# Kernel tuning notes

Measured on AMD Instinct MI355X. Metric: run time of the kernel, lower is better.

The kernel has to match this reference:

```python
import jax, jax.numpy as jnp
import numpy as np

# ---- static hyperparameters (mirror init_kwargs) ----
L_MAX = 3
N_MAX_L = [8, 6, 4, 2]            # radial basis size per l (precomputer.n_max_l)
N_CHANNELS = 32                   # num_element_channels
K_MAX_L = [n * N_CHANNELS for n in N_MAX_L]   # [256, 192, 128, 64]
SH_SIZES = [2 * l + 1 for l in range(L_MAX + 1)]  # [1,3,5,7]
MP_SCALING = 0.1
NU_SCALING = 0.1
NU_MAX = 2                        # max_correlation_order_per_layer
N_LAYERS = 2                      # num_message_passing_layers

# Fixed CG coupling tensors for all valid (l1, l2, L) with |l1-l2|<=L<=min(l1+l2, L_MAX).
# (Deterministic stand-ins for real Clebsch-Gordan coefficients; same sparsity/coupling
# structure and identical in fwd and fwdbwd modules.)
_rng = np.random.RandomState(0)
CG = {}
for _l1 in range(L_MAX + 1):
    for _l2 in range(L_MAX + 1):
        for _L in range(abs(_l1 - _l2), min(_l1 + _l2, L_MAX) + 1):
            CG[(_l1, _l2, _L)] = jnp.asarray(
                (_rng.randn(2 * _l1 + 1, 2 * _l2 + 1, 2 * _L + 1) * 0.2).astype(np.float32))


def split_l(x, sizes):
    out, i = [], 0
    for s in sizes:
        out.append(x[:, i:i + s])
        i += s
    return out


def embed_centers(feats, emb):
    # feats[l]: [N, 2l+1, n_l*C]; multiply channel block c by per-atom embedding emb[:, c]
    C = emb.shape[1]
    out = []
    for f in feats:
        n, m, k = f.shape
        out.append((f.reshape(n, m, k // C, C) * emb[:, None, None, :]).reshape(n, m, k))
    return out


def tensor_product(A, B):
    # per-atom CG tensor product, channel-aligned with truncation to min k
    n = A[0].shape[0]
    out = [jnp.zeros((n, 2 * L + 1, K_MAX_L[L]), A[0].dtype) for L in range(L_MAX + 1)]
    for (l1, l2, L), cg in CG.items():
        kk = min(K_MAX_L[l1], K_MAX_L[l2], K_MAX_L[L])
        t = jnp.einsum('nak,nbk,abM->nMk', A[l1][:, :, :kk], B[l2][:, :, :kk], cg)
        out[L] = out[L].at[:, :, :kk].add(t)
    return out


def cg_iterate(feats):
    # CGIterator: nu_max-1 iterated tensor products with residual accumulation
    g = feats
    for _ in range(NU_MAX - 1):
        tp = tensor_product(g, feats)
        g = [g[l] + NU_SCALING * tp[l] for l in range(L_MAX + 1)]
    return g


def invariant_mp(rb_l, sh_l, centers, emb_nbr, n_atoms):
    # spherical expansion: scatter rb x sh x neighbor-embedding over pairs -> centers
    out = []
    for l in range(L_MAX + 1):
        # [P, 2l+1, n_l, C] -> [P, 2l+1, k_l]
        msg = sh_l[l][:, :, None, None] * rb_l[l][:, None, :, None] * emb_nbr[:, None, None, :]
        msg = msg.reshape(msg.shape[0], 2 * l + 1, -1)
        out.append(MP_SCALING * jax.ops.segment_sum(msg, centers, num_segments=n_atoms))
    return out


def equivariant_mp(rb_l, sh_l, centers, neighbors, feats, n_atoms):
    # pair messages: CG-couple radially weighted SH edge features with neighbor features
    edge = [sh_l[l] * rb_l[l].sum(-1, keepdims=True) for l in range(L_MAX + 1)]  # [P, 2l+1]
    out = [jnp.zeros((n_atoms, 2 * L + 1, K_MAX_L[L]), feats[0].dtype) for L in range(L_MAX + 1)]
    for (l1, l2, L), cg in CG.items():
        kk = min(K_MAX_L[l2], K_MAX_L[L])
        w = jnp.einsum('pa,abM->pbM', edge[l1], cg)        # [P, 2l2+1, 2L+1]
        fg = feats[l2][neighbors, :, :kk]                   # gather: [P, 2l2+1, kk]
        msg = jnp.einsum('pbM,pbk->pMk', w, fg)             # [P, 2L+1, kk]
        out[L] = out[L].at[:, :, :kk].add(
            MP_SCALING * jax.ops.segment_sum(msg, centers, num_segments=n_atoms))
    return out


def setup_inputs() -> dict:
    key = jax.random.key(0)
    ks = jax.random.split(key, 8)
    N, P = 5000, 100000
    return {
        'sh': jax.random.normal(ks[0], (P, sum(SH_SIZES)), dtype=jnp.float32),
        'rb': jax.random.uniform(ks[1], (P, sum(N_MAX_L)), dtype=jnp.float32),
        'emb_table': jax.random.normal(ks[2], (4, N_CHANNELS), dtype=jnp.float32),
        'w_energy': jax.random.normal(ks[3], (K_MAX_L[0], 1), dtype=jnp.float32) * 0.05,
        'b_energy': jax.random.normal(ks[4], (1,), dtype=jnp.float32),
        'species_idx': jax.random.randint(ks[5], (N,), 0, 4, dtype=jnp.int32),
        'centers': jax.random.randint(ks[6], (P,), 0, N, dtype=jnp.int32),
        'neighbors': jax.random.randint(ks[7], (P,), 0, N, dtype=jnp.int32),
    }


def reference(sh, rb, emb_table, w_energy, b_energy, species_idx, centers, neighbors):
    n_atoms = species_idx.shape[0]
    sh_l = split_l(sh * NU_SCALING, SH_SIZES)   # nu_scaling applied to spherical harmonics
    rb_l = split_l(rb, N_MAX_L)
    center_emb = emb_table[species_idx]          # [N, C]
    emb_nbr = center_emb[neighbors]              # [P, C]
    # invariant message passing -> spherical expansion, then first CG iteration
    feats = invariant_mp(rb_l, sh_l, centers, emb_nbr, n_atoms)
    feats = cg_iterate(feats)
    # remaining equivariant message-passing layers
    for _ in range(N_LAYERS - 1):
        ef = embed_centers(feats, center_emb)
        mp = equivariant_mp(rb_l, sh_l, centers, neighbors, ef, n_atoms)
        feats = cg_iterate(mp)
    feats = embed_centers(feats, center_emb)
    energies = feats[0] @ w_energy + b_energy    # [N, 1, 1]
    return energies
```

## Files before the change

kernel.cpp:

```cpp
#include <hip/hip_runtime.h>
#include <vector>
#include <cmath>
#include <cstdint>

constexpr int KLc[4]  = {256,192,128,64};
constexpr int NMLc[4] = {8,6,4,2};
constexpr int SHBc[5] = {0,1,4,9,16};
constexpr int RBBc[5] = {0,8,14,18,20};
constexpr int FBc[5]  = {0,256,832,1472,1920};
constexpr int NCMB = 34, CGTOT = 3436, FTOT = 1920;

struct Combos { int l1[NCMB], l2[NCMB], L[NCMB], cgoff[NCMB], kk[NCMB]; };
constexpr Combos make_combos(){
  Combos c{}; int n=0, cg=0;
  for(int a=0;a<=3;a++)for(int b=0;b<=3;b++){
    int lo=a>b?a-b:b-a, hi=(a+b<3)?(a+b):3;
    for(int L=lo;L<=hi;L++){
      c.l1[n]=a; c.l2[n]=b; c.L[n]=L; c.cgoff[n]=cg;
      int mx=a>b?a:b; if(L>mx) mx=L; c.kk[n]=KLc[mx];
      cg+=(2*a+1)*(2*b+1)*(2*L+1); n++;
    }
  }
  return c;
}
constexpr Combos CB = make_combos();
static_assert(CB.cgoff[NCMB-1] + 7*7*7 == CGTOT, "cg size");

struct Grp { int cnt[4]; int list[4][12]; };
constexpr Grp make_Lg(){ Grp g{}; for(int i=0;i<NCMB;i++){ int L=CB.L[i]; g.list[L][g.cnt[L]++]=i; } return g; }
constexpr Grp LG = make_Lg();

struct Rows { int sh[64], rb[64], off[64]; };
constexpr Rows make_rows(){ Rows r{}; int i=0;
  for(int l=0;l<4;l++)for(int m=0;m<2*l+1;m++)for(int n=0;n<NMLc[l];n++){
    r.sh[i]=SHBc[l]+m; r.rb[i]=RBBc[l]+n; r.off[i]=FBc[l]+m*KLc[l]+n*32; i++; }
  for(;i<64;i++){ r.sh[i]=0; r.rb[i]=0; r.off[i]=0; }
  return r; }
constexpr Rows RWS = make_rows();

constexpr int NSL=425, NG=16, RPAD=149;
constexpr int JB=48, DEPTH=8;
static_assert(JB % DEPTH == 0, "slot rotation alignment");
constexpr int NTILE=30;

constexpr int iabs_(int x){ return x<0?-x:x; }
__host__ __device__ constexpr bool sl_valid(int l1,int l2,int kt){ return l2<=3-kt && iabs_(l1-l2)<=3-kt; }

__host__ __device__ constexpr int rb_base(int kt,int l1,int l2){
  int base=0;
  for(int p=0;p<4;p++)for(int q=0;q<4;q++){
    if(p==l1 && q==l2) return base;
    if(sl_valid(p,q,kt)) base += (2*p+1)*(2*q+1);
  }
  return base;
}

struct EqTab {
  short       srow[NG][32];
  signed char sph [NG][32];
  int nr[NG];
  short roff[NG][2];
  int total;
};
constexpr EqTab make_eqtab(){
  EqTab T{};
  for(int g=0;g<NG;g++){
    for(int s=0;s<32;s++){ T.srow[g][s]=-1; T.sph[g][s]=-1; }
    T.nr[g]=0; T.roff[g][0]=0; T.roff[g][1]=0;
  }
  int tl2[NTILE]{}, tkt[NTILE]{}, tbb[NTILE]{}, tsz[NTILE]{}; int nt=0;
  for(int l2=0;l2<4;l2++)for(int kt=0;kt<4-l2;kt++)for(int b=0;b<2*l2+1;b++){
    int sz=0;
    for(int l1=0;l1<4;l1++) if(sl_valid(l1,l2,kt)) sz+=2*l1+1;
    tl2[nt]=l2; tkt[nt]=kt; tbb[nt]=b; tsz[nt]=sz; nt++;
  }
  bool used[NTILE]{}; int gload[NG]{}; int gcnt[NG]{}; int gt[NG][2]{};
  for(int it=0; it<nt; it++){
    int best=-1;
    for(int i=0;i<nt;i++) if(!used[i] && (best<0 || tsz[i]>tsz[best])) best=i;
    used[best]=true;
    int g=-1;
    for(int j=0;j<NG;j++) if(gcnt[j]<2 && (g<0 || gload[j]<gload[g])) g=j;
    gt[g][gcnt[g]]=best; gcnt[g]++; gload[g]+=tsz[best];
  }
  int total=0;
  for(int g=0;g<NG;g++){
    T.nr[g]=gcnt[g];
    for(int tk=0;tk<gcnt[g];tk++){
      const int ti=gt[g][tk];
      const int l2=tl2[ti], kt=tkt[ti], b=tbb[ti];
      T.roff[g][tk]=(short)(FBc[l2]+b*KLc[l2]+kt*64);
      for(int i=0;i<16;i++){
        const int l1=(i==0)?0:(i<4)?1:(i<9)?2:3;
        const int aa=i-SHBc[l1];
        if(!sl_valid(l1,l2,kt)) continue;
        const int s=tk*16+i;
        const int rbi=rb_base(kt,l1,l2)+aa*(2*l2+1)+b;
        int ph, sr;
        if(kt==0){ if(l1<=2){ ph=0; sr=rbi; } else { ph=1; sr=rbi-144; } }
        else { ph=kt+1; sr=rbi; }
        T.sph[g][s]=(signed char)ph; T.srow[g][s]=(short)sr;
        total++;
      }
    }
    if(gcnt[g]==1) T.roff[g][1]=T.roff[g][0];
  }
  T.total=total;
  return T;
}
constexpr EqTab ET = make_eqtab();
static_assert(ET.total==NSL, "slice count");
constexpr bool chk_srow(){ for(int g=0;g<NG;g++) for(int s=0;s<32;s++) if(ET.srow[g][s]>=RPAD) return false; return true; }
static_assert(chk_srow(), "stage rows fit RPAD");

struct RoffA { int r0[NG]; int r1[NG]; };
constexpr RoffA make_roffa(){ RoffA R{}; for(int g=0;g<NG;g++){ R.r0[g]=ET.roff[g][0]; R.r1[g]=ET.roff[g][1]; } return R; }
constexpr RoffA RFA = make_roffa();

struct CAsg { int cnt[NG]; unsigned char ci[NG][8]; };
constexpr CAsg make_casg(){
  CAsg C{}; bool used[NCMB]{}; int load[NG]{};
  for(int it=0; it<NCMB; it++){
    int best=-1, bc=-1;
    for(int i=0;i<NCMB;i++) if(!used[i]){
      int c=(2*CB.l1[i]+1)*(2*CB.l2[i]+1)*(2*CB.L[i]+1);
      if(c>bc){bc=c;best=i;}
    }
    used[best]=true;
    int g=0; for(int j=1;j<NG;j++) if(load[j]<load[g]) g=j;
    C.ci[g][C.cnt[g]++]=(unsigned char)best; load[g]+=bc;
  }
  return C;
}
constexpr CAsg CA = make_casg();
constexpr bool chk_ca(){ for(int g=0;g<NG;g++) if(CA.cnt[g]>8) return false; return true; }
static_assert(chk_ca(), "CA cap");

__host__ __device__ constexpr bool combo_in_phase(int ci,int ph){
  int l1=CB.l1[ci], l2=CB.l2[ci], L=CB.L[ci];
  if(ph==0) return l1<=2;
  if(ph==1) return l1==3;
  int kt=ph-1;
  return (l2<=3-kt) && (L<=3-kt);
}
__host__ __device__ constexpr int phase_kt(int ph){ return ph<=1?0:ph-1; }
__host__ __device__ constexpr int phase_rbadj(int ph){ return ph==1?144:0; }

namespace nprng {
struct MT {
  uint32_t mt[624]; int mti; bool has_g; double g;
  void seed(uint32_t s){ for(int i=0;i<624;i++){ mt[i]=s; s=1812433253u*(s^(s>>30))+(uint32_t)i+1u; } mti=624; has_g=false; g=0.0; }
  uint32_t u32(){
    if(mti>=624){
      for(int i=0;i<624;i++){
        uint32_t y=(mt[i]&0x80000000u)|(mt[(i+1)%624]&0x7fffffffu);
        mt[i]=mt[(i+397)%624]^(y>>1)^((y&1u)?0x9908b0dfu:0u);
      }
      mti=0;
    }
    uint32_t y=mt[mti++];
    y^=y>>11; y^=(y<<7)&0x9d2c5680u; y^=(y<<15)&0xefc60000u; y^=y>>18;
    return y;
  }
  double dbl(){ uint32_t a=u32()>>5, b=u32()>>6; return (a*67108864.0+b)/9007199254740992.0; }
  double gauss(){
    if(has_g){ has_g=false; return g; }
    double f,x1,x2,r2;
    do{ x1=2.0*dbl()-1.0; x2=2.0*dbl()-1.0; r2=x1*x1+x2*x2; }while(r2>=1.0||r2==0.0);
    f=sqrt(-2.0*log(r2)/r2);
    g=f*x1; has_g=true; return f*x2;
  }
};
}
static std::vector<float> build_cg(){
  nprng::MT r; r.seed(0);
  std::vector<float> v; v.reserve(CGTOT);
  for(int l1=0;l1<=3;l1++)for(int l2=0;l2<=3;l2++){
    int lo = l1>l2? l1-l2 : l2-l1;
    int hi = (l1+l2<3)? (l1+l2) : 3;
    for(int L=lo;L<=hi;L++){
      int n=(2*l1+1)*(2*l2+1)*(2*L+1);
      for(int i=0;i<n;i++) v.push_back((float)(r.gauss()*0.2));
    }
  }
  return v;
}

__global__ __launch_bounds__(256) void k_cemb(const float* __restrict__ emb_table,
    const int* __restrict__ species, float* __restrict__ cemb, int* __restrict__ counts, int N){
  int i = blockIdx.x*256 + threadIdx.x;
  if(i < N) counts[i] = 0;
  if(i < N*32){ int n = i>>5, c = i&31; cemb[i] = emb_table[species[n]*32 + c]; }
}

__global__ __launch_bounds__(256) void k_hist(const int* __restrict__ centers, int* counts, int P){
  int i = blockIdx.x*256 + threadIdx.x;
  if(i < P) atomicAdd(&counts[centers[i]], 1);
}

__global__ __launch_bounds__(256) void k_scan(const int* __restrict__ counts,
    int* __restrict__ offsets, int* __restrict__ cursor, int N){
  __shared__ int part[256];
  const int t = threadIdx.x;
  const int CH = (N + 255)/256;
  const int lo = t*CH;
  int hi = (t+1)*CH; if(hi > N) hi = N;
  int s = 0;
  for(int i=lo;i<hi;i++) s += counts[i];
  part[t] = s; __syncthreads();
  const int own = s;
  for(int d=1; d<256; d<<=1){
    int v = (t>=d)? part[t-d] : 0;
    __syncthreads();
    part[t] += v;
    __syncthreads();
  }
  int run = part[t] - own;
  for(int i=lo;i<hi;i++){ offsets[i]=run; cursor[i]=run; run += counts[i]; }
  if(t==255) offsets[N] = part[255];
}

__global__ __launch_bounds__(256) void k_scatter(const int* __restrict__ centers,
    int* cursor, int* __restrict__ perm, int P){
  int i = blockIdx.x*256 + threadIdx.x;
  if(i < P){ int c = centers[i]; int pos = atomicAdd(&cursor[c], 1); perm[pos] = i; }
}

__global__ __launch_bounds__(256) void k_permute(const float* __restrict__ sh,
    const float* __restrict__ rb, const int* __restrict__ nbrs, const int* __restrict__ perm,
    float* __restrict__ edge_p, int* __restrict__ nbrp, int P){
  int u = blockIdx.x*256 + threadIdx.x;
  int pos = u>>4, i = u&15;
  if(pos >= P) return;
  int p = perm[pos];
  if(i==0) nbrp[pos] = nbrs[p];
  int l = (i==0)?0:(i<4)?1:(i<9)?2:3;
  float s=0.f;
  for(int n=RBBc[l]; n<RBBc[l+1]; n++) s += rb[p*20+n];
  edge_p[(size_t)pos*16+i] = sh[p*16+i]*0.1f*s;
}

__global__ __launch_bounds__(256) void k_inv(const float* __restrict__ sh, const float* __restrict__ rb,
    const float* __restrict__ cemb, const int* __restrict__ nbrs, const int* __restrict__ offsets,
    const int* __restrict__ perm, float* __restrict__ feats){
  const int a = blockIdx.x, t = threadIdx.x;
  __shared__ float sh_s[8][16], rb_s[8][20], emb_s[8][32], shrb_s[8][60];
  const int c = t & 31, rg = t >> 5;
  float acc[8];
  #pragma unroll
  for(int j=0;j<8;j++) acc[j] = 0.f;
  const int beg = offsets[a], cnt = offsets[a+1]-beg;
  for(int jb=0; jb<cnt; jb+=8){
    __syncthreads();
    for(int u=t; u<8*36; u+=256){
      int j=u/36, i=u-36*j;
      if(jb+j<cnt){
        int p=perm[beg+jb+j];
        if(i<16) sh_s[j][i]=sh[p*16+i]*0.1f;
        else     rb_s[j][i-16]=rb[p*20+i-16];
      }
    }
    for(int u=t; u<8*32; u+=256){
      int j=u>>5, i=u&31;
      if(jb+j<cnt){ int nb=nbrs[perm[beg+jb+j]]; emb_s[j][i]=cemb[(size_t)nb*32+i]; }
    }
    __syncthreads();
    for(int u=t; u<8*60; u+=256){
      int j=u/60, r=u-60*j;
      if(jb+j<cnt) shrb_s[j][r] = sh_s[j][RWS.sh[r]] * rb_s[j][RWS.rb[r]];
    }
    __syncthreads();
    const int jm = (cnt-jb<8)?(cnt-jb):8;
    for(int j=0;j<jm;j++){
      const float e = emb_s[j][c];
      #pragma unroll
      for(int q=0;q<8;q++){ int r=rg+8*q; if(r<60) acc[q]=fmaf(shrb_s[j][r], e, acc[q]); }
    }
  }
  #pragma unroll
  for(int q=0;q<8;q++){
    int r = rg + 8*q;
    if(r < 60) feats[(size_t)a*FTOT + RWS.off[r] + c] = 0.1f * acc[q];
  }
}

__device__ __forceinline__ float cg_u(const float* __restrict__ cg, int idx){
  return cg[__builtin_amdgcn_readfirstlane(idx)];
}
__global__ __launch_bounds__(256) void k_tp(float* __restrict__ feats, const float* __restrict__ cg){
  const int a = blockIdx.x, t = threadIdx.x;
  __shared__ float f_s[FTOT];
  float* fa = feats + (size_t)a*FTOT;
  for(int i=t;i<FTOT;i+=256)  f_s[i]  = fa[i];
  __syncthreads();
  #pragma unroll
  for(int L=0; L<4; L++){
    const int KLL = KLc[L], nL = 2*L+1;
    const int nel = nL*KLL;
    for(int e=t; e<nel; e+=256){
      const int M = e / KLL, k = e - M*KLL;
      float acc = 0.f;
      #pragma unroll
      for(int gi=0; gi<LG.cnt[L]; gi++){
        const int ci = LG.list[L][gi];
        const int l1 = CB.l1[ci], l2 = CB.l2[ci];
        if(k < CB.kk[ci]){
          const int n2 = 2*l2+1;
          #pragma unroll
          for(int aa=0; aa<2*l1+1; aa++){
            const float Av = f_s[FBc[l1] + aa*KLc[l1] + k];
            #pragma unroll
            for(int b=0; b<n2; b++)
              acc += cg_u(cg, CB.cgoff[ci] + (aa*n2+b)*nL + M) * (Av * f_s[FBc[l2] + b*KLc[l2] + k]);
          }
        }
      }
      fa[FBc[L] + M*KLL + k] = f_s[FBc[L] + M*KLL + k] + 0.1f*acc;
    }
  }
}

template<int G,int PH,int U>
__device__ __forceinline__ void contract_combos(const float* __restrict__ stageT,
    float* __restrict__ out_s, const float* __restrict__ cg, int lane){
  if constexpr (U < CA.cnt[G]) {
    constexpr int ci = CA.ci[G][U];
    if constexpr (combo_in_phase(ci,PH)) {
      constexpr int l1=CB.l1[ci], l2=CB.l2[ci], L=CB.L[ci];
      constexpr int n1=2*l1+1, n2=2*l2+1, nL=2*L+1;
      constexpr int kt=phase_kt(PH);
      constexpr int rbase = rb_base(kt,l1,l2) - phase_rbadj(PH);
      float oa[nL];
      #pragma unroll
      for(int M=0;M<nL;M++) oa[M]=0.f;
      #pragma unroll
      for(int aa=0;aa<n1;aa++){
        #pragma unroll
        for(int b=0;b<n2;b++){
          const float sv = stageT[lane*RPAD + rbase + aa*n2 + b];
          #pragma unroll
          for(int M=0;M<nL;M++)
            oa[M] = fmaf(cg[CB.cgoff[ci] + (aa*n2+b)*nL + M], sv, oa[M]);
        }
      }
      #pragma unroll
      for(int M=0;M<nL;M++)
        atomicAdd(&out_s[FBc[L] + M*KLc[L] + kt*64 + lane], oa[M]);
    }
    contract_combos<G,PH,U+1>(stageT,out_s,cg,lane);
  }
}

template<int G,int PH>
__device__ __forceinline__ void eq_phase(const float* acc, float* stageT, float* out_s,
    const float* __restrict__ cg, int lane){
  __syncthreads();
  #pragma unroll
  for(int s=0;s<32;s++){
    if(ET.sph[G][s]==PH) stageT[lane*RPAD + ET.srow[G][s]] = acc[s];
  }
  __syncthreads();
  contract_combos<G,PH,0>(stageT,out_s,cg,lane);
}

template<int G>
__device__ __forceinline__ void eq_phases(const float* acc, float* stageT, float* out_s,
    const float* __restrict__ cg, int lane){
  eq_phase<G,0>(acc,stageT,out_s,cg,lane);
  eq_phase<G,1>(acc,stageT,out_s,cg,lane);
  eq_phase<G,2>(acc,stageT,out_s,cg,lane);
  eq_phase<G,3>(acc,stageT,out_s,cg,lane);
  eq_phase<G,4>(acc,stageT,out_s,cg,lane);
}

__device__ __forceinline__ void eq_load_pair(float* fg, float& ce, int nb, int lane,
    int ro0, int ro1, const float* __restrict__ featsA, const float* __restrict__ cemb){
  ce = cemb[(size_t)nb*32 + (lane&31)];
  const float* fp = featsA + (size_t)nb*FTOT + lane;
  fg[0] = fp[ro0];
  fg[1] = fp[ro1];
}

__device__ __forceinline__ void eq_compute_pair(float* acc, const float* fg, float ce,
    const float* edge_row){
  float ed[16];
  #pragma unroll
  for(int q=0;q<4;q++){
    float4 v = *(const float4*)(edge_row + q*4);
    ed[q*4]=v.x; ed[q*4+1]=v.y; ed[q*4+2]=v.z; ed[q*4+3]=v.w;
  }
  const float f0 = fg[0]*ce, f1 = fg[1]*ce;
  #pragma unroll
  for(int i=0;i<16;i++) acc[i]    = fmaf(ed[i], f0, acc[i]);
  #pragma unroll
  for(int i=0;i<16;i++) acc[16+i] = fmaf(ed[i], f1, acc[16+i]);
}

__global__ __launch_bounds__(1024,4) void k_eq2(const float* __restrict__ edge_p,
    const int* __restrict__ nbrp, const float* __restrict__ cemb,
    const int* __restrict__ offsets, const float* __restrict__ featsA,
    float* __restrict__ featsB, const float* __restrict__ cg){
  __shared__ float stageT[64*RPAD];
  __shared__ float out_s[FTOT];
  __shared__ float edge_s[JB*16];
  __shared__ int   nb_s[JB];
  const int a = blockIdx.x, t = threadIdx.x, lane = t&63, g = t>>6;

  float acc[32];
  #pragma unroll
  for(int s=0;s<32;s++) acc[s]=0.f;
  for(int i=t;i<FTOT;i+=1024) out_s[i]=0.f;
  const int beg = offsets[a], cnt = offsets[a+1]-beg;
  const int ro0 = __builtin_amdgcn_readfirstlane(RFA.r0[g]);
  const int ro1 = __builtin_amdgcn_readfirstlane(RFA.r1[g]);

  float fgS[DEPTH][2]; float ceS[DEPTH];
  #pragma unroll
  for(int s=0;s<DEPTH;s++){
    int nb = (s<cnt)? nbrp[beg+s] : 0;
    eq_load_pair(fgS[s], ceS[s], nb, lane, ro0, ro1, featsA, cemb);
  }
  for(int jb=0; jb<cnt; jb+=JB){
    __syncthreads();
    if(t < JB*16){
      int j = t>>4;
      if(jb+j < cnt) edge_s[t] = edge_p[(size_t)(beg+jb)*16 + t];
    }
    if(t < JB) nb_s[t] = (jb+t < cnt) ? nbrp[beg+jb+t] : 0;
    __syncthreads();
    const int jm = (cnt-jb<JB)?(cnt-jb):JB;
    for(int j=0;j<jm;j+=DEPTH){
      #pragma unroll
      for(int s=0;s<DEPTH;s++){
        if(j+s < jm){
          eq_compute_pair(acc, fgS[s], ceS[s], edge_s + (j+s)*16);
          int q = jb+j+s+DEPTH;
          int nb = (q<cnt) ? ((q-jb<JB)? nb_s[q-jb] : nbrp[beg+q]) : 0;
          eq_load_pair(fgS[s], ceS[s], nb, lane, ro0, ro1, featsA, cemb);
        }
      }
    }
  }

  switch(g){
    case 0:  eq_phases<0 >(acc,stageT,out_s,cg,lane); break;
    case 1:  eq_phases<1 >(acc,stageT,out_s,cg,lane); break;
    case 2:  eq_phases<2 >(acc,stageT,out_s,cg,lane); break;
    case 3:  eq_phases<3 >(acc,stageT,out_s,cg,lane); break;
    case 4:  eq_phases<4 >(acc,stageT,out_s,cg,lane); break;
    case 5:  eq_phases<5 >(acc,stageT,out_s,cg,lane); break;
    case 6:  eq_phases<6 >(acc,stageT,out_s,cg,lane); break;
    case 7:  eq_phases<7 >(acc,stageT,out_s,cg,lane); break;
    case 8:  eq_phases<8 >(acc,stageT,out_s,cg,lane); break;
    case 9:  eq_phases<9 >(acc,stageT,out_s,cg,lane); break;
    case 10: eq_phases<10>(acc,stageT,out_s,cg,lane); break;
    case 11: eq_phases<11>(acc,stageT,out_s,cg,lane); break;
    case 12: eq_phases<12>(acc,stageT,out_s,cg,lane); break;
    case 13: eq_phases<13>(acc,stageT,out_s,cg,lane); break;
    case 14: eq_phases<14>(acc,stageT,out_s,cg,lane); break;
    default: eq_phases<15>(acc,stageT,out_s,cg,lane); break;
  }
  __syncthreads();
  float* ob = featsB + (size_t)a*FTOT;
  for(int i=t;i<FTOT;i+=1024) ob[i] = 0.1f*out_s[i];
}

__global__ __launch_bounds__(256) void k_energy(const float* __restrict__ feats,
    const float* __restrict__ cemb, const float* __restrict__ wE, const float* __restrict__ bE,
    float* __restrict__ out, int N){
  const int wid = threadIdx.x >> 6, lane = threadIdx.x & 63;
  const int a = blockIdx.x*4 + wid;
  if(a >= N) return;
  const float e = cemb[(size_t)a*32 + (lane & 31)];
  float s = 0.f;
  for(int k=lane; k<256; k+=64) s += feats[(size_t)a*FTOT + k] * e * wE[k];
  #pragma unroll
  for(int off=32; off; off>>=1) s += __shfl_down(s, off, 64);
  if(lane == 0) out[a] = s + bE[0];
}

extern "C" void kernel_launch(void* const* d_in, const int* in_sizes, int n_in,
                              void* d_out, int out_size, void* d_ws, size_t ws_size,
                              hipStream_t stream){
  const float* sh        = (const float*)d_in[0];
  const float* rb        = (const float*)d_in[1];
  const float* emb_table = (const float*)d_in[2];
  const float* wE        = (const float*)d_in[3];
  const float* bE        = (const float*)d_in[4];
  const int*   species   = (const int*)d_in[5];
  const int*   centers   = (const int*)d_in[6];
  const int*   nbrs      = (const int*)d_in[7];
  const int N = in_sizes[5];
  const int P = in_sizes[6];

  char* ws = (char*)d_ws; size_t off = 0;
  auto carve = [&](size_t bytes)->void*{
    void* p = ws + off; off = (off + bytes + 255) & ~(size_t)255; return p;
  };
  float* cg_d    = (float*)carve((size_t)CGTOT*4);
  float* cemb    = (float*)carve((size_t)N*32*4);
  int*   counts  = (int*)  carve((size_t)N*4);
  int*   offsets = (int*)  carve((size_t)(N+1)*4);
  int*   cursor  = (int*)  carve((size_t)N*4);
  int*   perm    = (int*)  carve((size_t)P*4);
  float* edge_pd = (float*)carve((size_t)P*16*4);
  int*   nbrp    = (int*)  carve((size_t)P*4);
  float* featsA  = (float*)carve((size_t)N*FTOT*4);
  float* featsB  = (float*)carve((size_t)N*FTOT*4);
  (void)ws_size; (void)n_in; (void)out_size;

  static const std::vector<float> cg_host = build_cg();
  hipMemcpyAsync(cg_d, cg_host.data(), (size_t)CGTOT*4, hipMemcpyHostToDevice, stream);

  k_cemb   <<<(N*32 + 255)/256, 256, 0, stream>>>(emb_table, species, cemb, counts, N);
  k_hist   <<<(P + 255)/256,    256, 0, stream>>>(centers, counts, P);
  k_scan   <<<1,                256, 0, stream>>>(counts, offsets, cursor, N);
  k_scatter<<<(P + 255)/256,    256, 0, stream>>>(centers, cursor, perm, P);
  k_permute<<<(P*16 + 255)/256, 256, 0, stream>>>(sh, rb, nbrs, perm, edge_pd, nbrp, P);
  k_inv    <<<N,                256, 0, stream>>>(sh, rb, cemb, nbrs, offsets, perm, featsA);
  k_tp     <<<N,                256, 0, stream>>>(featsA, cg_d);
  k_eq2    <<<N,               1024, 0, stream>>>(edge_pd, nbrp, cemb, offsets, featsA, featsB, cg_d);
  k_tp     <<<N,                256, 0, stream>>>(featsB, cg_d);
  k_energy <<<(N + 3)/4,        256, 0, stream>>>(featsB, cemb, wE, bE, (float*)d_out, N);
}
```

Measured before the change: 1.002 ms.

## Gather neighbor features as fp16 and pack species into neighbor index

Adds a conversion kernel that stores the first-layer features in half precision, so the equivariant message-passing kernel gathers neighbor features at half the bytes. The neighbor's species is packed into the upper bits of the permuted neighbor index, and the embedding table is cached in shared memory. This removes the per-edge global gather of center embeddings. It costs an extra conversion pass, loses precision in the features, and assumes fewer than 65536 atoms and that the species index selects a row of a 4x32 embedding table.

```diff
diff --git a/kernel.cpp b/kernel.cpp
--- a/kernel.cpp
+++ b/kernel.cpp
@@ -227,17 +227,26 @@
 }
 
 __global__ __launch_bounds__(256) void k_permute(const float* __restrict__ sh,
-    const float* __restrict__ rb, const int* __restrict__ nbrs, const int* __restrict__ perm,
-    float* __restrict__ edge_p, int* __restrict__ nbrp, int P){
+    const float* __restrict__ rb, const int* __restrict__ nbrs, const int* __restrict__ species,
+    const int* __restrict__ perm, float* __restrict__ edge_p, int* __restrict__ nbrp, int P){
   int u = blockIdx.x*256 + threadIdx.x;
   int pos = u>>4, i = u&15;
   if(pos >= P) return;
   int p = perm[pos];
-  if(i==0) nbrp[pos] = nbrs[p];
+  if(i==0){ int nb = nbrs[p]; nbrp[pos] = (species[nb]<<16) | nb; }
   int l = (i==0)?0:(i<4)?1:(i<9)?2:3;
   float s=0.f;
   for(int n=RBBc[l]; n<RBBc[l+1]; n++) s += rb[p*20+n];
   edge_p[(size_t)pos*16+i] = sh[p*16+i]*0.1f*s;
+}
+
+__global__ __launch_bounds__(256) void k_half(const float* __restrict__ src,
+    unsigned short* __restrict__ dst, int n){
+  int i = blockIdx.x*256 + threadIdx.x;
+  if(i < n){
+    _Float16 h = (_Float16)src[i];
+    dst[i] = *(unsigned short*)&h;
+  }
 }
 
 __global__ __launch_bounds__(256) void k_inv(const float* __restrict__ sh, const float* __restrict__ rb,
@@ -373,23 +382,23 @@
   eq_phase<G,4>(acc,stageT,out_s,cg,lane);
 }
 
-__device__ __forceinline__ void eq_load_pair(float* fg, float& ce, int nb, int lane,
-    int ro0, int ro1, const float* __restrict__ featsA, const float* __restrict__ cemb){
-  ce = cemb[(size_t)nb*32 + (lane&31)];
-  const float* fp = featsA + (size_t)nb*FTOT + lane;
+__device__ __forceinline__ void eq_load_pair(unsigned short* fg, int nbsp, int lane,
+    int ro0, int ro1, const unsigned short* __restrict__ featsAh){
+  const unsigned short* fp = featsAh + (size_t)(nbsp & 0xFFFF)*FTOT + lane;
   fg[0] = fp[ro0];
   fg[1] = fp[ro1];
 }
 
-__device__ __forceinline__ void eq_compute_pair(float* acc, const float* fg, float ce,
-    const float* edge_row){
+__device__ __forceinline__ void eq_compute_pair(float* acc, const unsigned short* fgh,
+    float ce, const float* edge_row){
   float ed[16];
   #pragma unroll
   for(int q=0;q<4;q++){
     float4 v = *(const float4*)(edge_row + q*4);
     ed[q*4]=v.x; ed[q*4+1]=v.y; ed[q*4+2]=v.z; ed[q*4+3]=v.w;
   }
-  const float f0 = fg[0]*ce, f1 = fg[1]*ce;
+  const float f0 = (float)(*(const _Float16*)&fgh[0]) * ce;
+  const float f1 = (float)(*(const _Float16*)&fgh[1]) * ce;
   #pragma unroll
   for(int i=0;i<16;i++) acc[i]    = fmaf(ed[i], f0, acc[i]);
   #pragma unroll
@@ -397,15 +406,17 @@
 }
 
 __global__ __launch_bounds__(1024,4) void k_eq2(const float* __restrict__ edge_p,
-    const int* __restrict__ nbrp, const float* __restrict__ cemb,
-    const int* __restrict__ offsets, const float* __restrict__ featsA,
+    const int* __restrict__ nbrp, const float* __restrict__ emb_table,
+    const int* __restrict__ offsets, const unsigned short* __restrict__ featsAh,
     float* __restrict__ featsB, const float* __restrict__ cg){
   __shared__ float stageT[64*RPAD];
   __shared__ float out_s[FTOT];
   __shared__ float edge_s[JB*16];
   __shared__ int   nb_s[JB];
+  __shared__ float semb_s[128];
   const int a = blockIdx.x, t = threadIdx.x, lane = t&63, g = t>>6;
 
+  if(t < 128) semb_s[t] = emb_table[t];
   float acc[32];
   #pragma unroll
   for(int s=0;s<32;s++) acc[s]=0.f;
@@ -413,12 +424,13 @@
   const int beg = offsets[a], cnt = offsets[a+1]-beg;
   const int ro0 = __builtin_amdgcn_readfirstlane(RFA.r0[g]);
   const int ro1 = __builtin_amdgcn_readfirstlane(RFA.r1[g]);
-
-  float fgS[DEPTH][2]; float ceS[DEPTH];
+  const int cidx = lane & 31;
+
+  unsigned short fgS[DEPTH][2];
   #pragma unroll
   for(int s=0;s<DEPTH;s++){
-    int nb = (s<cnt)? nbrp[beg+s] : 0;
-    eq_load_pair(fgS[s], ceS[s], nb, lane, ro0, ro1, featsA, cemb);
+    int v = (s<cnt)? nbrp[beg+s] : 0;
+    eq_load_pair(fgS[s], v, lane, ro0, ro1, featsAh);
   }
   for(int jb=0; jb<cnt; jb+=JB){
     __syncthreads();
@@ -433,10 +445,11 @@
       #pragma unroll
       for(int s=0;s<DEPTH;s++){
         if(j+s < jm){
-          eq_compute_pair(acc, fgS[s], ceS[s], edge_s + (j+s)*16);
+          const float ce = semb_s[((unsigned)nb_s[j+s]>>16)*32 + cidx];
+          eq_compute_pair(acc, fgS[s], ce, edge_s + (j+s)*16);
           int q = jb+j+s+DEPTH;
-          int nb = (q<cnt) ? ((q-jb<JB)? nb_s[q-jb] : nbrp[beg+q]) : 0;
-          eq_load_pair(fgS[s], ceS[s], nb, lane, ro0, ro1, featsA, cemb);
+          int v = (q<cnt) ? ((q-jb<JB)? nb_s[q-jb] : nbrp[beg+q]) : 0;
+          eq_load_pair(fgS[s], v, lane, ro0, ro1, featsAh);
         }
       }
     }
@@ -507,6 +520,7 @@
   int*   nbrp    = (int*)  carve((size_t)P*4);
   float* featsA  = (float*)carve((size_t)N*FTOT*4);
   float* featsB  = (float*)carve((size_t)N*FTOT*4);
+  unsigned short* featsAh = (unsigned short*)carve((size_t)N*FTOT*2);
   (void)ws_size; (void)n_in; (void)out_size;
 
   static const std::vector<float> cg_host = build_cg();
@@ -516,10 +530,11 @@
   k_hist   <<<(P + 255)/256,    256, 0, stream>>>(centers, counts, P);
   k_scan   <<<1,                256, 0, stream>>>(counts, offsets, cursor, N);
   k_scatter<<<(P + 255)/256,    256, 0, stream>>>(centers, cursor, perm, P);
-  k_permute<<<(P*16 + 255)/256, 256, 0, stream>>>(sh, rb, nbrs, perm, edge_pd, nbrp, P);
+  k_permute<<<(P*16 + 255)/256, 256, 0, stream>>>(sh, rb, nbrs, species, perm, edge_pd, nbrp, P);
   k_inv    <<<N,                256, 0, stream>>>(sh, rb, cemb, nbrs, offsets, perm, featsA);
   k_tp     <<<N,                256, 0, stream>>>(featsA, cg_d);
-  k_eq2    <<<N,               1024, 0, stream>>>(edge_pd, nbrp, cemb, offsets, featsA, featsB, cg_d);
+  k_half   <<<(N*FTOT + 255)/256, 256, 0, stream>>>(featsA, featsAh, N*FTOT);
+  k_eq2    <<<N,               1024, 0, stream>>>(edge_pd, nbrp, emb_table, offsets, featsAh, featsB, cg_d);
   k_tp     <<<N,                256, 0, stream>>>(featsB, cg_d);
   k_energy <<<(N + 3)/4,        256, 0, stream>>>(featsB, cemb, wE, bE, (float*)d_out, N);
 }
```

Result: no change. 1.008 ms (+0.6%).

## Pre-embed and pack neighbor features to fp16 pairs for equivariant gather

Applied to the files above, without the earlier changes.

Adds a kernel that multiplies layer-1 features by the center embedding and packs the two per-wave feature rows into one fp16x2 word per lane. The equivariant message-passing kernel then gathers a single 32-bit word per neighbor instead of two fp32 features plus an embedding value, cutting gather bandwidth and register use. It also hoists the first edge tile load, lowers the prefetch depth, and raises the occupancy hint. Rounding to fp16 reduces precision of the gathered features, and the extra pass adds a write and read of the packed buffer.

```diff
diff --git a/kernel.cpp b/kernel.cpp
--- a/kernel.cpp
+++ b/kernel.cpp
@@ -39,9 +39,10 @@
 constexpr Rows RWS = make_rows();
 
 constexpr int NSL=425, NG=16, RPAD=149;
-constexpr int JB=48, DEPTH=8;
+constexpr int JB=48, DEPTH=6;
 static_assert(JB % DEPTH == 0, "slot rotation alignment");
 constexpr int NTILE=30;
+constexpr int GSTR=1024;
 
 constexpr int iabs_(int x){ return x<0?-x:x; }
 __host__ __device__ constexpr bool sl_valid(int l1,int l2,int kt){ return l2<=3-kt && iabs_(l1-l2)<=3-kt; }
@@ -238,6 +239,20 @@
   float s=0.f;
   for(int n=RBBc[l]; n<RBBc[l+1]; n++) s += rb[p*20+n];
   edge_p[(size_t)pos*16+i] = sh[p*16+i]*0.1f*s;
+}
+
+__global__ __launch_bounds__(256) void k_halfg(const float* __restrict__ src,
+    const float* __restrict__ cemb, unsigned int* __restrict__ dst, int N){
+  int u = blockIdx.x*256 + threadIdx.x;
+  if(u >= N*GSTR) return;
+  int n = u >> 10, o = u & 1023;
+  int g = o >> 6, i = o & 63;
+  float c = cemb[n*32 + (i&31)];
+  float v0 = src[(size_t)n*FTOT + RFA.r0[g] + i] * c;
+  float v1 = src[(size_t)n*FTOT + RFA.r1[g] + i] * c;
+  _Float16 h0 = (_Float16)v0, h1 = (_Float16)v1;
+  unsigned int lo = *(unsigned short*)&h0, hi = *(unsigned short*)&h1;
+  dst[u] = lo | (hi<<16);
 }
 
 __global__ __launch_bounds__(256) void k_inv(const float* __restrict__ sh, const float* __restrict__ rb,
@@ -373,32 +388,27 @@
   eq_phase<G,4>(acc,stageT,out_s,cg,lane);
 }
 
-__device__ __forceinline__ void eq_load_pair(float* fg, float& ce, int nb, int lane,
-    int ro0, int ro1, const float* __restrict__ featsA, const float* __restrict__ cemb){
-  ce = cemb[(size_t)nb*32 + (lane&31)];
-  const float* fp = featsA + (size_t)nb*FTOT + lane;
-  fg[0] = fp[ro0];
-  fg[1] = fp[ro1];
-}
-
-__device__ __forceinline__ void eq_compute_pair(float* acc, const float* fg, float ce,
+__device__ __forceinline__ void eq_compute_pair(float* acc, unsigned int v,
     const float* edge_row){
-  float ed[16];
+  union { unsigned int u; _Float16 h[2]; } cv; cv.u = v;
+  const float f0 = (float)cv.h[0], f1 = (float)cv.h[1];
   #pragma unroll
   for(int q=0;q<4;q++){
-    float4 v = *(const float4*)(edge_row + q*4);
-    ed[q*4]=v.x; ed[q*4+1]=v.y; ed[q*4+2]=v.z; ed[q*4+3]=v.w;
-  }
-  const float f0 = fg[0]*ce, f1 = fg[1]*ce;
-  #pragma unroll
-  for(int i=0;i<16;i++) acc[i]    = fmaf(ed[i], f0, acc[i]);
-  #pragma unroll
-  for(int i=0;i<16;i++) acc[16+i] = fmaf(ed[i], f1, acc[16+i]);
-}
-
-__global__ __launch_bounds__(1024,4) void k_eq2(const float* __restrict__ edge_p,
-    const int* __restrict__ nbrp, const float* __restrict__ cemb,
-    const int* __restrict__ offsets, const float* __restrict__ featsA,
+    float4 e4 = *(const float4*)(edge_row + q*4);
+    acc[q*4+0]    = fmaf(e4.x, f0, acc[q*4+0]);
+    acc[q*4+1]    = fmaf(e4.y, f0, acc[q*4+1]);
+    acc[q*4+2]    = fmaf(e4.z, f0, acc[q*4+2]);
+    acc[q*4+3]    = fmaf(e4.w, f0, acc[q*4+3]);
+    acc[16+q*4+0] = fmaf(e4.x, f1, acc[16+q*4+0]);
+    acc[16+q*4+1] = fmaf(e4.y, f1, acc[16+q*4+1]);
+    acc[16+q*4+2] = fmaf(e4.z, f1, acc[16+q*4+2]);
+    acc[16+q*4+3] = fmaf(e4.w, f1, acc[16+q*4+3]);
+  }
+}
+
+__global__ __launch_bounds__(1024,8) void k_eq2(const float* __restrict__ edge_p,
+    const int* __restrict__ nbrp, const int* __restrict__ offsets,
+    const unsigned int* __restrict__ featsAg,
     float* __restrict__ featsB, const float* __restrict__ cg){
   __shared__ float stageT[64*RPAD];
   __shared__ float out_s[FTOT];
@@ -411,32 +421,40 @@
   for(int s=0;s<32;s++) acc[s]=0.f;
   for(int i=t;i<FTOT;i+=1024) out_s[i]=0.f;
   const int beg = offsets[a], cnt = offsets[a+1]-beg;
-  const int ro0 = __builtin_amdgcn_readfirstlane(RFA.r0[g]);
-  const int ro1 = __builtin_amdgcn_readfirstlane(RFA.r1[g]);
-
-  float fgS[DEPTH][2]; float ceS[DEPTH];
+  const int goff = g*64 + lane;
+
+  if(t < JB*16){
+    int j = t>>4;
+    if(j < cnt) edge_s[t] = edge_p[(size_t)beg*16 + t];
+  }
+  if(t < JB) nb_s[t] = (t < cnt) ? nbrp[beg+t] : 0;
+  __syncthreads();
+
+  unsigned int fgS[DEPTH];
   #pragma unroll
   for(int s=0;s<DEPTH;s++){
-    int nb = (s<cnt)? nbrp[beg+s] : 0;
-    eq_load_pair(fgS[s], ceS[s], nb, lane, ro0, ro1, featsA, cemb);
+    int nb = (s<cnt)? nb_s[s] : 0;
+    fgS[s] = featsAg[(size_t)nb*GSTR + goff];
   }
   for(int jb=0; jb<cnt; jb+=JB){
-    __syncthreads();
-    if(t < JB*16){
-      int j = t>>4;
-      if(jb+j < cnt) edge_s[t] = edge_p[(size_t)(beg+jb)*16 + t];
-    }
-    if(t < JB) nb_s[t] = (jb+t < cnt) ? nbrp[beg+jb+t] : 0;
-    __syncthreads();
+    if(jb > 0){
+      __syncthreads();
+      if(t < JB*16){
+        int j = t>>4;
+        if(jb+j < cnt) edge_s[t] = edge_p[(size_t)(beg+jb)*16 + t];
+      }
+      if(t < JB) nb_s[t] = (jb+t < cnt) ? nbrp[beg+jb+t] : 0;
+      __syncthreads();
+    }
     const int jm = (cnt-jb<JB)?(cnt-jb):JB;
     for(int j=0;j<jm;j+=DEPTH){
       #pragma unroll
       for(int s=0;s<DEPTH;s++){
         if(j+s < jm){
-          eq_compute_pair(acc, fgS[s], ceS[s], edge_s + (j+s)*16);
+          eq_compute_pair(acc, fgS[s], edge_s + (j+s)*16);
           int q = jb+j+s+DEPTH;
           int nb = (q<cnt) ? ((q-jb<JB)? nb_s[q-jb] : nbrp[beg+q]) : 0;
-          eq_load_pair(fgS[s], ceS[s], nb, lane, ro0, ro1, featsA, cemb);
+          fgS[s] = featsAg[(size_t)nb*GSTR + goff];
         }
       }
     }
@@ -507,6 +525,7 @@
   int*   nbrp    = (int*)  carve((size_t)P*4);
   float* featsA  = (float*)carve((size_t)N*FTOT*4);
   float* featsB  = (float*)carve((size_t)N*FTOT*4);
+  unsigned int* featsAg = (unsigned int*)carve((size_t)N*GSTR*4);
   (void)ws_size; (void)n_in; (void)out_size;
 
   static const std::vector<float> cg_host = build_cg();
@@ -519,7 +538,8 @@
   k_permute<<<(P*16 + 255)/256, 256, 0, stream>>>(sh, rb, nbrs, perm, edge_pd, nbrp, P);
   k_inv    <<<N,                256, 0, stream>>>(sh, rb, cemb, nbrs, offsets, perm, featsA);
   k_tp     <<<N,                256, 0, stream>>>(featsA, cg_d);
-  k_eq2    <<<N,               1024, 0, stream>>>(edge_pd, nbrp, cemb, offsets, featsA, featsB, cg_d);
+  k_halfg  <<<(N*GSTR + 255)/256, 256, 0, stream>>>(featsA, cemb, featsAg, N);
+  k_eq2    <<<N,               1024, 0, stream>>>(edge_pd, nbrp, offsets, featsAg, featsB, cg_d);
   k_tp     <<<N,                256, 0, stream>>>(featsB, cg_d);
   k_energy <<<(N + 3)/4,        256, 0, stream>>>(featsB, cemb, wE, bE, (float*)d_out, N);
 }
```

Result: faster. 980.4 us (-2.2%).
